# Kernel tuning notes

Hardware: AMD Instinct MI355X
Metric: run time of the kernel (lower is better)

Reference implementation:

```python
import jax, jax.numpy as jnp
import numpy as np

POWER = 2.0
EPS = jnp.float32(np.finfo(np.float32).eps)


def setup_inputs() -> dict:
    key = jax.random.key(0)
    k1, k2, k3 = jax.random.split(key, 3)
    B, P, S = 2, 131072, 512
    station_coords = jax.random.uniform(k1, (B, S, 2), dtype=jnp.float32)
    station_values = jax.random.normal(k2, (B, S), dtype=jnp.float32)
    grid_points = jax.random.uniform(k3, (B, P, 2), dtype=jnp.float32)
    return {
        "station_coords": station_coords,
        "station_values": station_values,
        "grid_points": grid_points,
    }


def reference(station_coords, station_values, grid_points):
    # grid_points: (B, P, 2); station_coords: (B, S, 2)
    diff = grid_points[:, :, None, :] - station_coords[:, None, :, :]  # (B, P, S, 2)
    distances = jnp.sqrt(jnp.sum(diff * diff, axis=-1))                # (B, P, S)
    distances = jnp.where(distances == 0, EPS, distances)
    weights = 1.0 / distances ** POWER                                  # (B, P, S)
    weights_sum = jnp.sum(weights, axis=-1)                             # (B, P)
    interpolated = jnp.sum(weights * station_values[:, None, :], axis=-1) / weights_sum
    return interpolated  # (B, P)
```

## Files before the change

### kernel.cpp

```cpp
#include <hip/hip_runtime.h>
#include <hip/hip_bf16.h>


#define BLOCK 256
#define S_MAX 512
#define GPT 2

__global__ __launch_bounds__(BLOCK) void idw_kernel(
    const float* __restrict__ station_coords,
    const float* __restrict__ station_values,
    const float* __restrict__ grid_points,
    float* __restrict__ out,
    int P, int S) {

    __shared__ float st[S_MAX * 3];

    const int b = blockIdx.y;
    const float2* __restrict__ sc2 = (const float2*)(station_coords) + (size_t)b * S;
    const float*  __restrict__ svb = station_values + (size_t)b * S;

    for (int i = threadIdx.x; i < S; i += BLOCK) {
        const float2 c = sc2[i];
        st[3 * i + 0] = c.x;
        st[3 * i + 1] = c.y;
        st[3 * i + 2] = svb[i];
    }
    __syncthreads();

    const int tid = blockIdx.x * BLOCK + threadIdx.x;
    const float4 g01 = ((const float4*)grid_points)[(size_t)b * (P / 2) + tid];
    const float gx0 = g01.x, gy0 = g01.y, gx1 = g01.z, gy1 = g01.w;

    constexpr float EPS  = 1.1920928955078125e-07f;
    constexpr float EPS2 = EPS * EPS;

    float wsum0 = 0.0f, vsum0 = 0.0f;
    float wsum1 = 0.0f, vsum1 = 0.0f;

    const float4* __restrict__ st4 = (const float4*)st;

    auto do_pair = [&](float ax, float ay, float av,
                       float bx, float by, float bv) {
        {
            const float dxa = gx0 - ax, dya = gy0 - ay;
            float a = fmaf(dxa, dxa, dya * dya);
            a = fmaxf(a, EPS2);
            const float dxb = gx0 - bx, dyb = gy0 - by;
            float bq = fmaf(dxb, dxb, dyb * dyb);
            bq = fmaxf(bq, EPS2);
            const float r = __builtin_amdgcn_rcpf(a * bq);
            wsum0 = fmaf(a + bq, r, wsum0);
            vsum0 = fmaf(fmaf(bv, a, av * bq), r, vsum0);
        }
        {
            const float dxa = gx1 - ax, dya = gy1 - ay;
            float a = fmaf(dxa, dxa, dya * dya);
            a = fmaxf(a, EPS2);
            const float dxb = gx1 - bx, dyb = gy1 - by;
            float bq = fmaf(dxb, dxb, dyb * dyb);
            bq = fmaxf(bq, EPS2);
            const float r = __builtin_amdgcn_rcpf(a * bq);
            wsum1 = fmaf(a + bq, r, wsum1);
            vsum1 = fmaf(fmaf(bv, a, av * bq), r, vsum1);
        }
    };

#pragma unroll 4
    for (int k = 0; k < S_MAX / 4; ++k) {
        const float4 f0 = st4[3 * k + 0];
        const float4 f1 = st4[3 * k + 1];
        const float4 f2 = st4[3 * k + 2];
        do_pair(f0.x, f0.y, f0.z, f0.w, f1.x, f1.y);
        do_pair(f1.z, f1.w, f2.x, f2.y, f2.z, f2.w);
    }

    const float r0 = vsum0 / wsum0;
    const float r1 = vsum1 / wsum1;
    ((float2*)out)[(size_t)b * (P / 2) + tid] = make_float2(r0, r1);
}

extern "C" void kernel_launch(void* const* d_in, const int* in_sizes, int n_in,
                              void* d_out, int out_size, void* d_ws, size_t ws_size,
                              hipStream_t stream) {
    const float* station_coords = (const float*)d_in[0];
    const float* station_values = (const float*)d_in[1];
    const float* grid_points    = (const float*)d_in[2];
    float* out = (float*)d_out;

    const int B = 2;
    const int S = in_sizes[1] / B;
    const int P = out_size / B;

    dim3 grid(P / (BLOCK * GPT), B);
    dim3 block(BLOCK);
    idw_kernel<<<grid, block, 0, stream>>>(station_coords, station_values,
                                           grid_points, out, P, S);
}
```

Measured before the change: 87.04 us.

## Process four grid points per thread using packed two-wide float math

```diff
diff --git a/kernel.cpp b/kernel.cpp
--- a/kernel.cpp
+++ b/kernel.cpp
@@ -2,9 +2,27 @@
 #include <hip/hip_bf16.h>
 
 
+typedef float v2f __attribute__((ext_vector_type(2)));
+
 #define BLOCK 256
 #define S_MAX 512
-#define GPT 2
+#define GPT 4
+
+static __device__ __forceinline__ v2f vfma(v2f a, v2f b, v2f c) {
+#if __has_builtin(__builtin_elementwise_fma)
+    return __builtin_elementwise_fma(a, b, c);
+#else
+    v2f r; r.x = fmaf(a.x, b.x, c.x); r.y = fmaf(a.y, b.y, c.y); return r;
+#endif
+}
+static __device__ __forceinline__ v2f vmax(v2f a, v2f b) {
+#if __has_builtin(__builtin_elementwise_max)
+    return __builtin_elementwise_max(a, b);
+#else
+    v2f r; r.x = fmaxf(a.x, b.x); r.y = fmaxf(a.y, b.y); return r;
+#endif
+}
+static __device__ __forceinline__ v2f splat(float s) { v2f r = {s, s}; return r; }
 
 __global__ __launch_bounds__(BLOCK) void idw_kernel(
     const float* __restrict__ station_coords,
@@ -28,41 +46,37 @@
     __syncthreads();
 
     const int tid = blockIdx.x * BLOCK + threadIdx.x;
-    const float4 g01 = ((const float4*)grid_points)[(size_t)b * (P / 2) + tid];
-    const float gx0 = g01.x, gy0 = g01.y, gx1 = g01.z, gy1 = g01.w;
+    const float4* __restrict__ gp =
+        (const float4*)(grid_points + (size_t)b * P * 2);
+    const float4 gA = gp[2 * tid + 0];
+    const float4 gB = gp[2 * tid + 1];
+    const v2f gx01 = {gA.x, gA.z}, gy01 = {gA.y, gA.w};
+    const v2f gx23 = {gB.x, gB.z}, gy23 = {gB.y, gB.w};
 
     constexpr float EPS  = 1.1920928955078125e-07f;
-    constexpr float EPS2 = EPS * EPS;
+    const v2f eps2 = splat(EPS * EPS);
 
-    float wsum0 = 0.0f, vsum0 = 0.0f;
-    float wsum1 = 0.0f, vsum1 = 0.0f;
+    v2f wsum01 = {0.f, 0.f}, vsum01 = {0.f, 0.f};
+    v2f wsum23 = {0.f, 0.f}, vsum23 = {0.f, 0.f};
 
     const float4* __restrict__ st4 = (const float4*)st;
 
-    auto do_pair = [&](float ax, float ay, float av,
+    auto do_pair = [&](v2f gx, v2f gy, v2f& wsum, v2f& vsum,
+                       float ax, float ay, float av,
                        float bx, float by, float bv) {
-        {
-            const float dxa = gx0 - ax, dya = gy0 - ay;
-            float a = fmaf(dxa, dxa, dya * dya);
-            a = fmaxf(a, EPS2);
-            const float dxb = gx0 - bx, dyb = gy0 - by;
-            float bq = fmaf(dxb, dxb, dyb * dyb);
-            bq = fmaxf(bq, EPS2);
-            const float r = __builtin_amdgcn_rcpf(a * bq);
-            wsum0 = fmaf(a + bq, r, wsum0);
-            vsum0 = fmaf(fmaf(bv, a, av * bq), r, vsum0);
-        }
-        {
-            const float dxa = gx1 - ax, dya = gy1 - ay;
-            float a = fmaf(dxa, dxa, dya * dya);
-            a = fmaxf(a, EPS2);
-            const float dxb = gx1 - bx, dyb = gy1 - by;
-            float bq = fmaf(dxb, dxb, dyb * dyb);
-            bq = fmaxf(bq, EPS2);
-            const float r = __builtin_amdgcn_rcpf(a * bq);
-            wsum1 = fmaf(a + bq, r, wsum1);
-            vsum1 = fmaf(fmaf(bv, a, av * bq), r, vsum1);
-        }
+        const v2f dxa = gx - ax, dya = gy - ay;
+        v2f a = vfma(dxa, dxa, dya * dya);
+        a = vmax(a, eps2);
+        const v2f dxb = gx - bx, dyb = gy - by;
+        v2f bb = vfma(dxb, dxb, dyb * dyb);
+        bb = vmax(bb, eps2);
+        const v2f ab = a * bb;
+        v2f r;
+        r.x = __builtin_amdgcn_rcpf(ab.x);
+        r.y = __builtin_amdgcn_rcpf(ab.y);
+        wsum = vfma(a + bb, r, wsum);
+        const v2f vnum = vfma(splat(bv), a, splat(av) * bb);
+        vsum = vfma(vnum, r, vsum);
     };
 
 #pragma unroll 4
@@ -70,13 +84,18 @@
         const float4 f0 = st4[3 * k + 0];
         const float4 f1 = st4[3 * k + 1];
         const float4 f2 = st4[3 * k + 2];
-        do_pair(f0.x, f0.y, f0.z, f0.w, f1.x, f1.y);
-        do_pair(f1.z, f1.w, f2.x, f2.y, f2.z, f2.w);
+        do_pair(gx01, gy01, wsum01, vsum01, f0.x, f0.y, f0.z, f0.w, f1.x, f1.y);
+        do_pair(gx23, gy23, wsum23, vsum23, f0.x, f0.y, f0.z, f0.w, f1.x, f1.y);
+        do_pair(gx01, gy01, wsum01, vsum01, f1.z, f1.w, f2.x, f2.y, f2.z, f2.w);
+        do_pair(gx23, gy23, wsum23, vsum23, f1.z, f1.w, f2.x, f2.y, f2.z, f2.w);
     }
 
-    const float r0 = vsum0 / wsum0;
-    const float r1 = vsum1 / wsum1;
-    ((float2*)out)[(size_t)b * (P / 2) + tid] = make_float2(r0, r1);
+    float4 res;
+    res.x = vsum01.x / wsum01.x;
+    res.y = vsum01.y / wsum01.y;
+    res.z = vsum23.x / wsum23.x;
+    res.w = vsum23.y / wsum23.y;
+    ((float4*)out)[(size_t)b * (P / 4) + tid] = res;
 }
 
 extern "C" void kernel_launch(void* const* d_in, const int* in_sizes, int n_in,
```

Result: faster. 84.39 us (-3.0%).
